# Performance work log

Measured on AMD Instinct MI355X. Metric: run time of the kernel, lower is better.

The kernel has to match this reference:

```python
import jax, jax.numpy as jnp
import numpy as np

N_NODES = 100000
N_EDGES = 3200000
IN_DIM = 128
EMB = 32
NUM_GRAPHS = 256


def setup_inputs() -> dict:
    key = jax.random.key(0)
    ks = jax.random.split(key, 7)
    x = jax.random.normal(ks[0], (N_NODES, IN_DIM), dtype=jnp.float32)
    edge_index = jax.random.randint(ks[1], (2, N_EDGES), 0, N_NODES, dtype=jnp.int64)
    batch_index = jnp.sort(jax.random.randint(ks[2], (N_NODES,), 0, NUM_GRAPHS, dtype=jnp.int64))
    W1 = jax.random.normal(ks[3], (IN_DIM, EMB), dtype=jnp.float32) * (1.0 / np.sqrt(IN_DIM))
    b1 = jax.random.normal(ks[4], (EMB,), dtype=jnp.float32) * 0.01
    Wout = jax.random.normal(ks[5], (2 * EMB, 1), dtype=jnp.float32) * (1.0 / np.sqrt(2 * EMB))
    bout = jax.random.normal(ks[6], (1,), dtype=jnp.float32) * 0.01
    return {"x": x, "edge_index": edge_index, "batch_index": batch_index,
            "W1": W1, "b1": b1, "Wout": Wout, "bout": bout}


def gcn_conv(x, edge_index, W, b):
    """PyG GCNConv: add self-loops, symmetric deg^-1/2 normalization, XW, scatter-add, +bias."""
    N = x.shape[0]
    xw = x @ W  # [N, out]
    src, dst = edge_index[0], edge_index[1]
    # degree includes self-loop (+1)
    deg = jax.ops.segment_sum(jnp.ones(src.shape[0], dtype=xw.dtype), dst, num_segments=N) + 1.0
    dinv = jax.lax.rsqrt(deg)  # deg >= 1 so safe
    norm = dinv[src] * dinv[dst]  # [E]
    msg = xw[src] * norm[:, None]  # [E, out]
    agg = jax.ops.segment_sum(msg, dst, num_segments=N)
    # self-loop contribution: dinv[i]^2 * xw[i]
    agg = agg + xw * (dinv * dinv)[:, None]
    return agg + b


def reference(x, edge_index, batch_index, W1, b1, Wout, bout):
    h = gcn_conv(x, edge_index, W1, b1)           # [N, EMB]
    h = jnp.tanh(h)
    sums = jax.ops.segment_sum(h, batch_index, num_segments=NUM_GRAPHS)   # global_add_pool
    counts = jax.ops.segment_sum(jnp.ones((h.shape[0],), dtype=h.dtype), batch_index, num_segments=NUM_GRAPHS)
    means = sums / jnp.maximum(counts, 1.0)[:, None]                       # global_mean_pool
    pooled = jnp.concatenate([sums, means], axis=1)  # [G, 2*EMB]
    return pooled @ Wout + bout                      # [G, 1]
```

## Files before the change

### kernel.cpp

```cpp
#include <hip/hip_runtime.h>
#include <hip/hip_fp16.h>

#define N_NODES    100000
#define N_EDGES    3200000
#define IN_DIM     128
#define EMB        32
#define NUM_GRAPHS 256

#define FB         1024
#define NODES_PB   128
#define NBUCKETS   782
#define FB_B       512
#define FB_EPB     6250
#define NCHUNK     16
#define CHROWS     32
#define XW_BLOCKS  1563
#define CAP        5632

typedef _Float16 half8 __attribute__((ext_vector_type(8)));
typedef float floatx4 __attribute__((ext_vector_type(4)));

__global__ __launch_bounds__(512) void k_hist(const int* __restrict__ ei,
                                              int* __restrict__ bhist) {
    __shared__ int h[FB];
    int t = threadIdx.x;
    for (int i = t; i < FB; i += 512) h[i] = 0;
    __syncthreads();
    int e0 = blockIdx.x * FB_EPB;
    for (int e = e0 + t; e < e0 + FB_EPB; e += 512)
        atomicAdd(&h[ei[N_EDGES + e] >> 7], 1);
    __syncthreads();
    for (int i = t; i < FB; i += 512) bhist[blockIdx.x * FB + i] = h[i];
}

__global__ __launch_bounds__(512) void k_part(const int* __restrict__ bhist,
                                              int* __restrict__ part) {
    int j = blockIdx.x, t = threadIdx.x;
    int row0 = j * CHROWS;
    for (int b = t; b < FB; b += 512) {
        int acc = 0;
#pragma unroll 8
        for (int i = 0; i < CHROWS; ++i) acc += bhist[(row0 + i) * FB + b];
        part[j * FB + b] = acc;
    }
}

__global__ __launch_bounds__(1024) void k_mid(const int* __restrict__ bhist,
                                              const int* __restrict__ part,
                                              int* __restrict__ bbase,
                                              int* __restrict__ cbase) {
    __shared__ int ts[FB];
    int b = threadIdx.x;
    int j = blockIdx.x;
    int tot = 0;
#pragma unroll
    for (int k = 0; k < NCHUNK; ++k) tot += part[k * FB + b];
    ts[b] = tot;
    __syncthreads();
    for (int off = 1; off < FB; off <<= 1) {
        int u = (b >= off) ? ts[b - off] : 0;
        __syncthreads();
        ts[b] += u;
        __syncthreads();
    }
    int cb = ts[b] - tot;
    if (j == 0) {
        cbase[b] = cb;
        if (b == 0) cbase[FB] = N_EDGES;
    }
    int run = cb;
    for (int k = 0; k < j; ++k) run += part[k * FB + b];
    int row0 = j * CHROWS;
    for (int i = 0; i < CHROWS; ++i) {
        int h = bhist[(row0 + i) * FB + b];
        bbase[(row0 + i) * FB + b] = run;
        run += h;
    }
}

__global__ __launch_bounds__(512) void k_aux2(const int* __restrict__ batch,
                                              float* __restrict__ sums,
                                              float* __restrict__ counts) {
    int t = threadIdx.x;
    for (int i = t; i < NUM_GRAPHS * EMB; i += 512) sums[i] = 0.f;
    if (t < NUM_GRAPHS) {
        int lo = 0, hi = N_NODES;
        while (lo < hi) { int mid = (lo + hi) >> 1; if (batch[mid] < t) lo = mid + 1; else hi = mid; }
        int a = lo;
        lo = 0; hi = N_NODES;
        int g1 = t + 1;
        while (lo < hi) { int mid = (lo + hi) >> 1; if (batch[mid] < g1) lo = mid + 1; else hi = mid; }
        counts[t] = (float)(lo - a);
    }
}

__global__ __launch_bounds__(512) void k_fill(const int* __restrict__ ei,
                                              const int* __restrict__ bbase,
                                              unsigned int* __restrict__ recs) {
    __shared__ int lcur[FB];
    int t = threadIdx.x;
    for (int i = t; i < FB; i += 512) lcur[i] = bbase[blockIdx.x * FB + i];
    __syncthreads();
    int e0 = blockIdx.x * FB_EPB;
    for (int e = e0 + t; e < e0 + FB_EPB; e += 512) {
        int s = ei[e];
        int d = ei[N_EDGES + e];
        int b = d >> 7;
        int pos = atomicAdd(&lcur[b], 1);
        recs[pos] = ((unsigned int)(d & 127) << 24) | (unsigned int)s;
    }
}

__global__ __launch_bounds__(512) void k_fill2(const unsigned int* __restrict__ recs,
                                               const int* __restrict__ cbase,
                                               int* __restrict__ edge_src,
                                               int* __restrict__ rowstart,
                                               float* __restrict__ dinv) {
    __shared__ unsigned int lbuf[CAP];
    __shared__ int h2[NODES_PB], cur2[NODES_PB], sc[NODES_PB];
    int t = threadIdx.x, b = blockIdx.x;
    if (t < NODES_PB) h2[t] = 0;
    __syncthreads();
    int seg0 = cbase[b];
    int cnt = cbase[b + 1] - seg0;
    for (int j = t; j < cnt; j += 512) {
        unsigned int r = recs[seg0 + j];
        if (j < CAP) lbuf[j] = r;
        atomicAdd(&h2[r >> 24], 1);
    }
    __syncthreads();
    int v = 0;
    if (t < NODES_PB) { v = h2[t]; sc[t] = v; }
    __syncthreads();
    for (int off = 1; off < NODES_PB; off <<= 1) {
        int u = 0;
        if (t < NODES_PB && t >= off) u = sc[t - off];
        __syncthreads();
        if (t < NODES_PB) sc[t] += u;
        __syncthreads();
    }
    int node0 = b << 7;
    if (t < NODES_PB) {
        int excl = sc[t] - v;
        cur2[t] = excl;
        int node = node0 + t;
        if (node < N_NODES) {
            rowstart[node] = seg0 + excl;
            dinv[node] = rsqrtf((float)v + 1.0f);
        }
    }
    if (b == 0 && t == 0) rowstart[N_NODES] = N_EDGES;
    __syncthreads();
    for (int j = t; j < cnt; j += 512) {
        unsigned int r = (j < CAP) ? lbuf[j] : recs[seg0 + j];
        int p = atomicAdd(&cur2[r >> 24], 1);
        edge_src[seg0 + p] = (int)(r & 0x00FFFFFF);
    }
}

__global__ __launch_bounds__(256) void k_xw(const float* __restrict__ x,
                                            const float* __restrict__ W1,
                                            const float* __restrict__ dinv,
                                            __half* __restrict__ xwh) {
    __shared__ _Float16 Wh[IN_DIM * (EMB + 1)];
    for (int i = threadIdx.x; i < IN_DIM * EMB; i += 256)
        Wh[(i >> 5) * (EMB + 1) + (i & 31)] = (_Float16)W1[i];
    __syncthreads();
    int wave = threadIdx.x >> 6;
    int lane = threadIdx.x & 63;
    int m = lane & 15, quad = lane >> 4;
    int row0 = (blockIdx.x * 4 + wave) * 16;
    if (row0 >= N_NODES) return;
    half8 bfrag[2][4];
#pragma unroll
    for (int nt = 0; nt < 2; ++nt)
#pragma unroll
        for (int ks = 0; ks < 4; ++ks)
#pragma unroll
            for (int j = 0; j < 8; ++j)
                bfrag[nt][ks][j] = Wh[(ks * 32 + quad * 8 + j) * (EMB + 1) + nt * 16 + m];
    const float* xr = x + (size_t)(row0 + m) * IN_DIM + quad * 8;
    floatx4 c0 = {0.f, 0.f, 0.f, 0.f}, c1 = {0.f, 0.f, 0.f, 0.f};
#pragma unroll
    for (int ks = 0; ks < 4; ++ks) {
        float4 a0 = *(const float4*)(xr + ks * 32);
        float4 a1 = *(const float4*)(xr + ks * 32 + 4);
        half8 af;
        af[0] = (_Float16)a0.x; af[1] = (_Float16)a0.y;
        af[2] = (_Float16)a0.z; af[3] = (_Float16)a0.w;
        af[4] = (_Float16)a1.x; af[5] = (_Float16)a1.y;
        af[6] = (_Float16)a1.z; af[7] = (_Float16)a1.w;
        c0 = __builtin_amdgcn_mfma_f32_16x16x32_f16(af, bfrag[0][ks], c0, 0, 0, 0);
        c1 = __builtin_amdgcn_mfma_f32_16x16x32_f16(af, bfrag[1][ks], c1, 0, 0, 0);
    }
#pragma unroll
    for (int r = 0; r < 4; ++r) {
        int ro = row0 + quad * 4 + r;
        float di = dinv[ro];
        xwh[(size_t)ro * EMB + m]      = __float2half(c0[r] * di);
        xwh[(size_t)ro * EMB + 16 + m] = __float2half(c1[r] * di);
    }
}

template<int K>
__device__ __forceinline__ void gstep(const int* __restrict__ es,
                                      const __half2* __restrict__ rows,
                                      int cc, int e, float& a0, float& a1) {
    int s[K];
    float2 f[K];
#pragma unroll
    for (int k = 0; k < K; ++k) s[k] = es[e + k];
#pragma unroll
    for (int k = 0; k < K; ++k) f[k] = __half22float2(rows[s[k] * 16 + cc]);
#pragma unroll
    for (int k = 0; k < K; ++k) { a0 += f[k].x; a1 += f[k].y; }
}

__global__ __launch_bounds__(256) void k_gather(const __half* __restrict__ xws,
                                                const float* __restrict__ dinv,
                                                const int* __restrict__ rowstart,
                                                const int* __restrict__ edge_src,
                                                const int* __restrict__ batch,
                                                const float* __restrict__ b1,
                                                float* __restrict__ sums) {
    const __half2* rows = (const __half2*)xws;
    int grp = threadIdx.x >> 4;
    int cc  = threadIdx.x & 15;
    int i = blockIdx.x * 16 + grp;
    float di = dinv[i];
    int e0 = rowstart[i], e1 = rowstart[i + 1];
    float a0 = 0.f, a1 = 0.f;
    int e = e0;
    for (; e + 16 <= e1; e += 16) gstep<16>(edge_src, rows, cc, e, a0, a1);
    if (e + 8 <= e1) { gstep<8>(edge_src, rows, cc, e, a0, a1); e += 8; }
    if (e + 4 <= e1) { gstep<4>(edge_src, rows, cc, e, a0, a1); e += 4; }
    if (e + 2 <= e1) { gstep<2>(edge_src, rows, cc, e, a0, a1); e += 2; }
    if (e < e1)      { gstep<1>(edge_src, rows, cc, e, a0, a1); }
    float2 fs = __half22float2(rows[i * 16 + cc]);
    float2 bb = *(const float2*)(b1 + 2 * cc);
    float h0 = tanhf((a0 + fs.x) * di + bb.x);
    float h1 = tanhf((a1 + fs.y) * di + bb.y);

    __shared__ float hs[16][EMB];
    __shared__ int gb[16];
    *(float2*)&hs[grp][2 * cc] = make_float2(h0, h1);
    if (cc == 0) gb[grp] = batch[i];
    __syncthreads();
    if (threadIdx.x < 32) {
        int col = threadIdx.x;
        int rr = 0;
        while (rr < 16) {
            int g0 = gb[rr];
            float a = hs[rr][col];
            int r2 = rr + 1;
            while (r2 < 16 && gb[r2] == g0) { a += hs[r2][col]; ++r2; }
            atomicAdd(&sums[g0 * EMB + col], a);
            rr = r2;
        }
    }
}

__global__ __launch_bounds__(64) void k_out(const float* __restrict__ sums,
                                            const float* __restrict__ counts,
                                            const float* __restrict__ Wout,
                                            const float* __restrict__ bout,
                                            float* __restrict__ out) {
    int g = blockIdx.x * 64 + threadIdx.x;
    if (g >= NUM_GRAPHS) return;
    float inv = 1.0f / fmaxf(counts[g], 1.0f);
    float acc = bout[0];
#pragma unroll
    for (int c = 0; c < EMB; ++c) {
        float s = sums[g * EMB + c];
        acc += s * Wout[c] + s * inv * Wout[EMB + c];
    }
    out[g] = acc;
}

extern "C" void kernel_launch(void* const* d_in, const int* in_sizes, int n_in,
                              void* d_out, int out_size, void* d_ws, size_t ws_size,
                              hipStream_t stream) {
    const float* x     = (const float*)d_in[0];
    const int*   ei    = (const int*)d_in[1];
    const int*   batch = (const int*)d_in[2];
    const float* W1    = (const float*)d_in[3];
    const float* b1    = (const float*)d_in[4];
    const float* Wout  = (const float*)d_in[5];
    const float* bout  = (const float*)d_in[6];
    float* out = (float*)d_out;

    char* ws = (char*)d_ws;
    __half* xwh        = (__half*)ws;       ws += (size_t)N_NODES * EMB * sizeof(__half);
    unsigned int* recs = (unsigned int*)ws; ws += (size_t)N_EDGES * sizeof(int);
    int*   edge_src    = (int*)ws;          ws += (size_t)N_EDGES * sizeof(int);
    int*   rowstart    = (int*)ws;          ws += (size_t)(N_NODES + 4) * sizeof(int);
    float* dinv        = (float*)ws;        ws += (size_t)N_NODES * sizeof(float);
    int*   cbase       = (int*)ws;          ws += (FB + 2) * sizeof(int);
    float* sums        = (float*)ws;        ws += (size_t)NUM_GRAPHS * EMB * sizeof(float);
    float* counts      = (float*)ws;

    int* bhist = edge_src;
    int* part  = edge_src + (size_t)FB_B * FB;
    int* bbase = part + (size_t)NCHUNK * FB;

    k_aux2  <<<1, 512, 0, stream>>>(batch, sums, counts);
    k_hist  <<<FB_B, 512, 0, stream>>>(ei, bhist);
    k_part  <<<NCHUNK, 512, 0, stream>>>(bhist, part);
    k_mid   <<<NCHUNK, 1024, 0, stream>>>(bhist, part, bbase, cbase);
    k_fill  <<<FB_B, 512, 0, stream>>>(ei, bbase, recs);
    k_fill2 <<<NBUCKETS, 512, 0, stream>>>(recs, cbase, edge_src, rowstart, dinv);
    k_xw    <<<XW_BLOCKS, 256, 0, stream>>>(x, W1, dinv, xwh);
    k_gather<<<N_NODES / 16, 256, 0, stream>>>(xwh, dinv, rowstart, edge_src, batch, b1, sums);
    k_out   <<<(NUM_GRAPHS + 63) / 64, 64, 0, stream>>>(sums, counts, Wout, bout, out);
}
```

Before: 227.4 us.

## Stage bucket scatter in LDS for coalesced writes; fold aux kernel into k_part

```diff
diff --git a/kernel.cpp b/kernel.cpp
--- a/kernel.cpp
+++ b/kernel.cpp
@@ -34,8 +34,24 @@
 }
 
 __global__ __launch_bounds__(512) void k_part(const int* __restrict__ bhist,
-                                              int* __restrict__ part) {
+                                              int* __restrict__ part,
+                                              const int* __restrict__ batch,
+                                              float* __restrict__ sums,
+                                              float* __restrict__ counts) {
     int j = blockIdx.x, t = threadIdx.x;
+    if (j == NCHUNK) {
+        for (int i = t; i < NUM_GRAPHS * EMB; i += 512) sums[i] = 0.f;
+        if (t < NUM_GRAPHS) {
+            int lo = 0, hi = N_NODES;
+            while (lo < hi) { int mid = (lo + hi) >> 1; if (batch[mid] < t) lo = mid + 1; else hi = mid; }
+            int a = lo;
+            lo = 0; hi = N_NODES;
+            int g1 = t + 1;
+            while (lo < hi) { int mid = (lo + hi) >> 1; if (batch[mid] < g1) lo = mid + 1; else hi = mid; }
+            counts[t] = (float)(lo - a);
+        }
+        return;
+    }
     int row0 = j * CHROWS;
     for (int b = t; b < FB; b += 512) {
         int acc = 0;
@@ -78,37 +94,48 @@
     }
 }
 
-__global__ __launch_bounds__(512) void k_aux2(const int* __restrict__ batch,
-                                              float* __restrict__ sums,
-                                              float* __restrict__ counts) {
-    int t = threadIdx.x;
-    for (int i = t; i < NUM_GRAPHS * EMB; i += 512) sums[i] = 0.f;
-    if (t < NUM_GRAPHS) {
-        int lo = 0, hi = N_NODES;
-        while (lo < hi) { int mid = (lo + hi) >> 1; if (batch[mid] < t) lo = mid + 1; else hi = mid; }
-        int a = lo;
-        lo = 0; hi = N_NODES;
-        int g1 = t + 1;
-        while (lo < hi) { int mid = (lo + hi) >> 1; if (batch[mid] < g1) lo = mid + 1; else hi = mid; }
-        counts[t] = (float)(lo - a);
-    }
-}
-
 __global__ __launch_bounds__(512) void k_fill(const int* __restrict__ ei,
+                                              const int* __restrict__ bhist,
                                               const int* __restrict__ bbase,
                                               unsigned int* __restrict__ recs) {
-    __shared__ int lcur[FB];
+    __shared__ unsigned int staged[FB_EPB];
+    __shared__ int dpos[FB_EPB];
+    __shared__ int hd[FB];
+    __shared__ int cur[FB];
+    __shared__ int ts[512];
     int t = threadIdx.x;
-    for (int i = t; i < FB; i += 512) lcur[i] = bbase[blockIdx.x * FB + i];
+    int rowoff = blockIdx.x * FB;
+    for (int i = t; i < FB; i += 512) hd[i] = bhist[rowoff + i];
+    __syncthreads();
+    int v0 = hd[2 * t], v1 = hd[2 * t + 1];
+    int tot = v0 + v1;
+    ts[t] = tot;
+    __syncthreads();
+    for (int off = 1; off < 512; off <<= 1) {
+        int u = (t >= off) ? ts[t - off] : 0;
+        __syncthreads();
+        ts[t] += u;
+        __syncthreads();
+    }
+    int lb0 = ts[t] - tot;
+    int lb1 = lb0 + v0;
+    cur[2 * t] = lb0;
+    cur[2 * t + 1] = lb1;
+    hd[2 * t]     = bbase[rowoff + 2 * t]     - lb0;
+    hd[2 * t + 1] = bbase[rowoff + 2 * t + 1] - lb1;
     __syncthreads();
     int e0 = blockIdx.x * FB_EPB;
     for (int e = e0 + t; e < e0 + FB_EPB; e += 512) {
         int s = ei[e];
         int d = ei[N_EDGES + e];
         int b = d >> 7;
-        int pos = atomicAdd(&lcur[b], 1);
-        recs[pos] = ((unsigned int)(d & 127) << 24) | (unsigned int)s;
-    }
+        int lpos = atomicAdd(&cur[b], 1);
+        staged[lpos] = ((unsigned int)(d & 127) << 24) | (unsigned int)s;
+        dpos[lpos] = lpos + hd[b];
+    }
+    __syncthreads();
+    for (int j = t; j < FB_EPB; j += 512)
+        recs[dpos[j]] = staged[j];
 }
 
 __global__ __launch_bounds__(512) void k_fill2(const unsigned int* __restrict__ recs,
@@ -303,11 +330,10 @@
     int* part  = edge_src + (size_t)FB_B * FB;
     int* bbase = part + (size_t)NCHUNK * FB;
 
-    k_aux2  <<<1, 512, 0, stream>>>(batch, sums, counts);
     k_hist  <<<FB_B, 512, 0, stream>>>(ei, bhist);
-    k_part  <<<NCHUNK, 512, 0, stream>>>(bhist, part);
+    k_part  <<<NCHUNK + 1, 512, 0, stream>>>(bhist, part, batch, sums, counts);
     k_mid   <<<NCHUNK, 1024, 0, stream>>>(bhist, part, bbase, cbase);
-    k_fill  <<<FB_B, 512, 0, stream>>>(ei, bbase, recs);
+    k_fill  <<<FB_B, 512, 0, stream>>>(ei, bhist, bbase, recs);
     k_fill2 <<<NBUCKETS, 512, 0, stream>>>(recs, cbase, edge_src, rowstart, dinv);
     k_xw    <<<XW_BLOCKS, 256, 0, stream>>>(x, W1, dinv, xwh);
     k_gather<<<N_NODES / 16, 256, 0, stream>>>(xwh, dinv, rowstart, edge_src, batch, b1, sums);
```

Result: faster. 203.5 us (-10.5%).
